# Optimization experiments

Measured on AMD Instinct MI355X. Metric: run time of the kernel, lower is better.

## Reference

```python
import jax, jax.numpy as jnp
import numpy as np

IMG_W = 256
IMG_H = 256
N_PTS = 320
MIN_D = 2.0
MAX_D = 6.0
FOCAL = 2.0          # f = 1/tan(fov/2), fov ~ 53 deg
EPS_EA = 1e-10       # pytorch3d EmissionAbsorption eps
EPS = 1e-8           # module's normalization eps
DENSITY = 0.1        # constant density used when opacity is None


def trilinear_sample(vol, pts):
    """grid_sample-style trilinear, align_corners=True, zero padding.
    vol: (D,H,W); pts: (...,3) local coords (x->W, y->H, z->D) in [-1,1]."""
    D, H, W = vol.shape
    x, y, z = pts[..., 0], pts[..., 1], pts[..., 2]
    ix = (x + 1.0) * 0.5 * (W - 1)
    iy = (y + 1.0) * 0.5 * (H - 1)
    iz = (z + 1.0) * 0.5 * (D - 1)
    x0f, y0f, z0f = jnp.floor(ix), jnp.floor(iy), jnp.floor(iz)
    fx, fy, fz = ix - x0f, iy - y0f, iz - z0f
    x0 = x0f.astype(jnp.int32); x1 = x0 + 1
    y0 = y0f.astype(jnp.int32); y1 = y0 + 1
    z0 = z0f.astype(jnp.int32); z1 = z0 + 1
    out = jnp.zeros_like(ix)
    for zi, wz in ((z0, 1.0 - fz), (z1, fz)):
        for yi, wy in ((y0, 1.0 - fy), (y1, fy)):
            for xi, wx in ((x0, 1.0 - fx), (x1, fx)):
                valid = (xi >= 0) & (xi < W) & (yi >= 0) & (yi < H) & (zi >= 0) & (zi < D)
                v = vol[jnp.clip(zi, 0, D - 1), jnp.clip(yi, 0, H - 1), jnp.clip(xi, 0, W - 1)]
                out = out + jnp.where(valid, v * (wz * wy * wx), 0.0)
    return out


def setup_inputs() -> dict:
    key = jax.random.key(0)
    image3d = jax.random.uniform(key, (1, 1, 256, 256, 256), dtype=jnp.float32)
    R = jnp.eye(3, dtype=jnp.float32)[None]                 # (1,3,3) extrinsic rotation
    T = jnp.array([[0.0, 0.0, 4.0]], dtype=jnp.float32)     # (1,3) camera at z=-4 world
    return {"image3d": image3d, "R": R, "T": T}


def reference(image3d, R, T):
    B, C, D, H, W = image3d.shape
    vol = image3d[:, 0]                                     # (B,D,H,W); RGB repeat -> channels equal
    shape = max(C, D)
    vox = 3.0 / shape
    # --- NDC ray sampling (uniform depths) ---
    yg, xg = jnp.meshgrid(jnp.linspace(-1.0, 1.0, IMG_H),
                          jnp.linspace(-1.0, 1.0, IMG_W), indexing='ij')   # (IH,IW)
    depths = jnp.linspace(MIN_D, MAX_D, N_PTS)
    xcam = xg[..., None] * depths / FOCAL                   # (IH,IW,P)
    ycam = yg[..., None] * depths / FOCAL
    zcam = jnp.broadcast_to(depths, xcam.shape)
    pcam = jnp.stack([xcam, ycam, zcam], axis=-1)           # (IH,IW,P,3)
    # world points: X_cam = X_world @ R + T  =>  X_world = (X_cam - T) @ R^T
    v = pcam[None] - T[:, None, None, None, :]              # (B,IH,IW,P,3)
    pw = jnp.einsum('bhwpj,bkj->bhwpk', v, R)
    # world -> volume local coords (align_corners=True span over voxel centers)
    half = jnp.array([vox * (W - 1) * 0.5, vox * (H - 1) * 0.5, vox * (D - 1) * 0.5], jnp.float32)
    local = pw / half                                       # (B,IH,IW,P,3)
    # --- trilinear gather of features & densities ---
    feat = jax.vmap(trilinear_sample)(vol, local)           # (B,IH,IW,P)
    ones_vol = jnp.ones((D, H, W), jnp.float32)
    sigma = DENSITY * jax.vmap(trilinear_sample, in_axes=(None, 0))(ones_vol, local)
    # --- emission-absorption front-to-back compositing ---
    t = (1.0 + EPS_EA) - sigma
    absorption = jnp.cumprod(t, axis=-1)
    absorption = jnp.concatenate([jnp.ones_like(absorption[..., :1]), absorption[..., :-1]], axis=-1)
    weights = sigma * absorption
    rgb = jnp.sum(weights * feat, axis=-1)                  # (B,IH,IW); RGB channels identical
    # permute(0,3,2,1) then mean over 3 identical RGB channels -> (B,1,IW,IH)
    out = jnp.transpose(rgb, (0, 2, 1))[:, None]
    # norm_type == 'standardized': normalized(standardized(x))
    s = (out - out.mean()) / (jnp.std(out, ddof=1) + EPS)
    out = (s - s.min() + EPS) / (s.max() - s.min() + EPS)
    return out
```

## Files before the change

### kernel.cpp

```cpp
#include <hip/hip_runtime.h>

#define IMG 256
#define NPTS 320
#define NCHUNK 8
#define CHUNK (NPTS / NCHUNK)
#define PIX_PER_BLOCK 64
#define D0 2.0f
#define DSTEP (4.0f / 319.0f)
#define HALFV (765.0f / 512.0f)
#define DENSITY_C 0.1f

__global__ void render_kernel(const float* __restrict__ vol,
                              const float* __restrict__ R,
                              const float* __restrict__ T,
                              float* __restrict__ raw,
                              float* __restrict__ bsum,
                              float* __restrict__ bsumsq,
                              float* __restrict__ bmin,
                              float* __restrict__ bmax) {
  const int lane  = threadIdx.x & 63;
  const int chunk = threadIdx.x >> 6;
  const int pixel = blockIdx.x * PIX_PER_BLOCK + lane;
  const int h = pixel >> 8;
  const int w = pixel & 255;

  const float xh = (w * (2.0f / 255.0f) - 1.0f) * 0.5f;
  const float yh = (h * (2.0f / 255.0f) - 1.0f) * 0.5f;

  const float R00 = R[0], R01 = R[1], R02 = R[2];
  const float R10 = R[3], R11 = R[4], R12 = R[5];
  const float R20 = R[6], R21 = R[7], R22 = R[8];
  const float T0 = T[0], T1 = T[1], T2 = T[2];

  const float S = 127.5f / HALFV;
  const float Cx = R00 * xh + R01 * yh + R02;
  const float Cy = R10 * xh + R11 * yh + R12;
  const float Cz = R20 * xh + R21 * yh + R22;
  const float Kx = -(R00 * T0 + R01 * T1 + R02 * T2);
  const float Ky = -(R10 * T0 + R11 * T1 + R12 * T2);
  const float Kz = -(R20 * T0 + R21 * T1 + R22 * T2);
  const float ax = Cx * S, bx = Kx * S + 127.5f;
  const float ay = Cy * S, by = Ky * S + 127.5f;
  const float az = Cz * S, bz = Kz * S + 127.5f;
  const float ix0 = ax * D0 + bx, dix = ax * DSTEP;
  const float iy0 = ay * D0 + by, diy = ay * DSTEP;
  const float iz0 = az * D0 + bz, diz = az * DSTEP;

  float acc = 0.0f;
  float Tac = 1.0f;
  const int p0 = chunk * CHUNK;

  for (int i = 0; i < CHUNK; ++i) {
    const float pf = (float)(p0 + i);
    const float ix = fmaf(pf, dix, ix0);
    const float iy = fmaf(pf, diy, iy0);
    const float iz = fmaf(pf, diz, iz0);
    if (ix > -1.0f && ix < 256.0f && iy > -1.0f && iy < 256.0f &&
        iz > -1.0f && iz < 256.0f) {
      const float xf = floorf(ix), yf = floorf(iy), zf = floorf(iz);
      const float fx = ix - xf, fy = iy - yf, fz = iz - zf;
      const int x0 = (int)xf, y0 = (int)yf, z0 = (int)zf;
      const float wx0 = (x0 >= 0)   ? 1.0f - fx : 0.0f;
      const float wx1 = (x0 <= 254) ? fx        : 0.0f;
      const float wy0 = (y0 >= 0)   ? 1.0f - fy : 0.0f;
      const float wy1 = (y0 <= 254) ? fy        : 0.0f;
      const float wz0 = (z0 >= 0)   ? 1.0f - fz : 0.0f;
      const float wz1 = (z0 <= 254) ? fz        : 0.0f;
      const int xc0 = max(x0, 0),     xc1 = min(x0 + 1, 255);
      const int yc0 = max(y0, 0),     yc1 = min(y0 + 1, 255);
      const int zc0 = max(z0, 0),     zc1 = min(z0 + 1, 255);
      const int b00 = (zc0 * 256 + yc0) * 256;
      const int b01 = (zc0 * 256 + yc1) * 256;
      const int b10 = (zc1 * 256 + yc0) * 256;
      const int b11 = (zc1 * 256 + yc1) * 256;
      const float v000 = vol[b00 + xc0], v001 = vol[b00 + xc1];
      const float v010 = vol[b01 + xc0], v011 = vol[b01 + xc1];
      const float v100 = vol[b10 + xc0], v101 = vol[b10 + xc1];
      const float v110 = vol[b11 + xc0], v111 = vol[b11 + xc1];
      const float fs =
          wz0 * (wy0 * (wx0 * v000 + wx1 * v001) +
                 wy1 * (wx0 * v010 + wx1 * v011)) +
          wz1 * (wy0 * (wx0 * v100 + wx1 * v101) +
                 wy1 * (wx0 * v110 + wx1 * v111));
      const float wsum  = (wx0 + wx1) * (wy0 + wy1) * (wz0 + wz1);
      const float sigma = DENSITY_C * wsum;
      acc = fmaf(sigma * Tac, fs, acc);
      Tac *= (1.0f + 1e-10f - sigma);
    } else {
      Tac *= (1.0f + 1e-10f);
    }
  }

  __shared__ float lrgb[NCHUNK][PIX_PER_BLOCK];
  __shared__ float lT[NCHUNK][PIX_PER_BLOCK];
  lrgb[chunk][lane] = acc;
  lT[chunk][lane]   = Tac;
  __syncthreads();

  if (threadIdx.x < 64) {
    float a = 0.0f, Tp = 1.0f;
#pragma unroll
    for (int c = 0; c < NCHUNK; ++c) {
      a  = fmaf(Tp, lrgb[c][lane], a);
      Tp *= lT[c][lane];
    }
    raw[pixel] = a;

    float s = a, q = a * a, mn = a, mx = a;
#pragma unroll
    for (int off = 32; off > 0; off >>= 1) {
      s += __shfl_down(s, off, 64);
      q += __shfl_down(q, off, 64);
      mn = fminf(mn, __shfl_down(mn, off, 64));
      mx = fmaxf(mx, __shfl_down(mx, off, 64));
    }
    if (lane == 0) {
      bsum[blockIdx.x]   = s;
      bsumsq[blockIdx.x] = q;
      bmin[blockIdx.x]   = mn;
      bmax[blockIdx.x]   = mx;
    }
  }
}

__global__ void stats_kernel(const float* __restrict__ bsum,
                             const float* __restrict__ bsumsq,
                             const float* __restrict__ bmin,
                             const float* __restrict__ bmax,
                             float* __restrict__ stats) {
  __shared__ double sS[256], sQ[256];
  __shared__ float sMn[256], sMx[256];
  const int t = threadIdx.x;
  double s = 0.0, q = 0.0;
  float mn = 3.4e38f, mx = -3.4e38f;
  for (int i = t; i < 1024; i += 256) {
    s += (double)bsum[i];
    q += (double)bsumsq[i];
    mn = fminf(mn, bmin[i]);
    mx = fmaxf(mx, bmax[i]);
  }
  sS[t] = s; sQ[t] = q; sMn[t] = mn; sMx[t] = mx;
  __syncthreads();
  for (int off = 128; off > 0; off >>= 1) {
    if (t < off) {
      sS[t] += sS[t + off];
      sQ[t] += sQ[t + off];
      sMn[t] = fminf(sMn[t], sMn[t + off]);
      sMx[t] = fmaxf(sMx[t], sMx[t + off]);
    }
    __syncthreads();
  }
  if (t == 0) {
    const double N = 65536.0;
    const double mean = sS[0] / N;
    double var = (sQ[0] - sS[0] * sS[0] / N) / (N - 1.0);
    if (var < 0.0) var = 0.0;
    const float stdeps = (float)sqrt(var) + 1e-8f;
    const float fmean = (float)mean;
    const float smin = (sMn[0] - fmean) / stdeps;
    const float smax = (sMx[0] - fmean) / stdeps;
    stats[0] = fmean;
    stats[1] = 1.0f / stdeps;
    stats[2] = smin;
    stats[3] = 1.0f / (smax - smin + 1e-8f);
  }
}

__global__ void finalize_kernel(const float* __restrict__ raw,
                                const float* __restrict__ stats,
                                float* __restrict__ out) {
  const int o = blockIdx.x * blockDim.x + threadIdx.x;
  const int wq = o >> 8;
  const int hq = o & 255;
  const float mean = stats[0], inv_std = stats[1];
  const float smin = stats[2], inv_range = stats[3];
  const float s = (raw[hq * 256 + wq] - mean) * inv_std;
  out[o] = (s - smin + 1e-8f) * inv_range;
}

extern "C" void kernel_launch(void* const* d_in, const int* in_sizes, int n_in,
                              void* d_out, int out_size, void* d_ws, size_t ws_size,
                              hipStream_t stream) {
  const float* vol = (const float*)d_in[0];
  const float* R   = (const float*)d_in[1];
  const float* T   = (const float*)d_in[2];
  float* out = (float*)d_out;

  float* raw    = (float*)d_ws;
  float* bsum   = raw + 65536;
  float* bsumsq = bsum + 1024;
  float* bmin   = bsumsq + 1024;
  float* bmax   = bmin + 1024;
  float* stats  = bmax + 1024;

  render_kernel<<<1024, 512, 0, stream>>>(vol, R, T, raw, bsum, bsumsq, bmin, bmax);
  stats_kernel<<<1, 256, 0, stream>>>(bsum, bsumsq, bmin, bmax, stats);
  finalize_kernel<<<256, 256, 0, stream>>>(raw, stats, out);
}
```

Baseline: 131.1 us.

## Precompute ray-box intervals for a branch-free interior loop; fuse stats into finalize

Each ray's entry and exit sample indices against the volume are computed analytically with slab tests. Fully-interior samples then run a branchless trilinear loop with no bounds checks or weight masking. Only the boundary samples use the masked path, and samples fully outside are skipped. The stats reduction is also merged into the finalize kernel, with every block redoing the reduction, which removes one launch. The risks are numerical edge cases near the slab margins and the redundant per-block reduction.

```diff
diff --git a/kernel.cpp b/kernel.cpp
--- a/kernel.cpp
+++ b/kernel.cpp
@@ -1,6 +1,5 @@
 #include <hip/hip_runtime.h>
 
-#define IMG 256
 #define NPTS 320
 #define NCHUNK 8
 #define CHUNK (NPTS / NCHUNK)
@@ -10,14 +9,15 @@
 #define HALFV (765.0f / 512.0f)
 #define DENSITY_C 0.1f
 
-__global__ void render_kernel(const float* __restrict__ vol,
-                              const float* __restrict__ R,
-                              const float* __restrict__ T,
-                              float* __restrict__ raw,
-                              float* __restrict__ bsum,
-                              float* __restrict__ bsumsq,
-                              float* __restrict__ bmin,
-                              float* __restrict__ bmax) {
+__global__ __launch_bounds__(512, 8)
+void render_kernel(const float* __restrict__ vol,
+                   const float* __restrict__ R,
+                   const float* __restrict__ T,
+                   float* __restrict__ raw,
+                   float* __restrict__ bsum,
+                   float* __restrict__ bsumsq,
+                   float* __restrict__ bmin,
+                   float* __restrict__ bmax) {
   const int lane  = threadIdx.x & 63;
   const int chunk = threadIdx.x >> 6;
   const int pixel = blockIdx.x * PIX_PER_BLOCK + lane;
@@ -46,12 +46,34 @@
   const float iy0 = ay * D0 + by, diy = ay * DSTEP;
   const float iz0 = az * D0 + bz, diz = az * DSTEP;
 
+  float plo_in = -1e9f, phi_in = 1e9f, plo_out = -1e9f, phi_out = 1e9f;
+  auto slab = [](float a, float b, float L, float H, float& lo, float& hi) {
+    if (fabsf(a) < 1e-5f) {
+      if (b < L || b > H) { lo = 1e9f; hi = -1e9f; }
+    } else {
+      const float p1 = (L - b) / a, p2 = (H - b) / a;
+      lo = fmaxf(lo, fminf(p1, p2));
+      hi = fminf(hi, fmaxf(p1, p2));
+    }
+  };
+  slab(dix, ix0, 0.01f, 254.99f, plo_in, phi_in);
+  slab(diy, iy0, 0.01f, 254.99f, plo_in, phi_in);
+  slab(diz, iz0, 0.01f, 254.99f, plo_in, phi_in);
+  slab(dix, ix0, -1.01f, 256.01f, plo_out, phi_out);
+  slab(diy, iy0, -1.01f, 256.01f, plo_out, phi_out);
+  slab(diz, iz0, -1.01f, 256.01f, plo_out, phi_out);
+
+  const int i_in_lo  = (int)ceilf(fminf(fmaxf(plo_in, 0.0f), 320.0f));
+  const int i_in_hi  = (int)floorf(fminf(fmaxf(phi_in, -1.0f), 319.0f)) + 1;
+  const int i_out_lo = (int)ceilf(fminf(fmaxf(plo_out, 0.0f), 320.0f));
+  const int i_out_hi = (int)floorf(fminf(fmaxf(phi_out, -1.0f), 319.0f)) + 1;
+
   float acc = 0.0f;
   float Tac = 1.0f;
   const int p0 = chunk * CHUNK;
 
-  for (int i = 0; i < CHUNK; ++i) {
-    const float pf = (float)(p0 + i);
+  auto masked_sample = [&](int p) {
+    const float pf = (float)p;
     const float ix = fmaf(pf, dix, ix0);
     const float iy = fmaf(pf, diy, iy0);
     const float iz = fmaf(pf, diz, iz0);
@@ -89,7 +111,42 @@
     } else {
       Tac *= (1.0f + 1e-10f);
     }
+  };
+
+  const int lo_o = max(p0, i_out_lo);
+  const int hi_o = min(p0 + CHUNK, i_out_hi);
+  const int lo_f = min(max(lo_o, i_in_lo), hi_o);
+  const int hi_f = min(max(lo_f, i_in_hi), hi_o);
+
+  for (int p = lo_o; p < lo_f; ++p) masked_sample(p);
+
+#pragma unroll 4
+  for (int p = lo_f; p < hi_f; ++p) {
+    const float pf = (float)p;
+    const float ix = fmaf(pf, dix, ix0);
+    const float iy = fmaf(pf, diy, iy0);
+    const float iz = fmaf(pf, diz, iz0);
+    const int x0 = (int)ix, y0 = (int)iy, z0 = (int)iz;
+    const float fx = ix - (float)x0;
+    const float fy = iy - (float)y0;
+    const float fz = iz - (float)z0;
+    const int base = (z0 << 16) + (y0 << 8) + x0;
+    const float v000 = vol[base],         v001 = vol[base + 1];
+    const float v010 = vol[base + 256],   v011 = vol[base + 257];
+    const float v100 = vol[base + 65536], v101 = vol[base + 65537];
+    const float v110 = vol[base + 65792], v111 = vol[base + 65793];
+    const float c00 = fmaf(fx, v001 - v000, v000);
+    const float c01 = fmaf(fx, v011 - v010, v010);
+    const float c10 = fmaf(fx, v101 - v100, v100);
+    const float c11 = fmaf(fx, v111 - v110, v110);
+    const float c0  = fmaf(fy, c01 - c00, c00);
+    const float c1  = fmaf(fy, c11 - c10, c10);
+    const float fs  = fmaf(fz, c1 - c0, c0);
+    acc = fmaf(Tac * DENSITY_C, fs, acc);
+    Tac *= (1.0f - DENSITY_C);
   }
+
+  for (int p = hi_f; p < hi_o; ++p) masked_sample(p);
 
   __shared__ float lrgb[NCHUNK][PIX_PER_BLOCK];
   __shared__ float lT[NCHUNK][PIX_PER_BLOCK];
@@ -123,25 +180,23 @@
   }
 }
 
-__global__ void stats_kernel(const float* __restrict__ bsum,
-                             const float* __restrict__ bsumsq,
-                             const float* __restrict__ bmin,
-                             const float* __restrict__ bmax,
-                             float* __restrict__ stats) {
-  __shared__ double sS[256], sQ[256];
-  __shared__ float sMn[256], sMx[256];
+__global__ __launch_bounds__(1024)
+void finalize_kernel(const float* __restrict__ raw,
+                     const float* __restrict__ bsum,
+                     const float* __restrict__ bsumsq,
+                     const float* __restrict__ bmin,
+                     const float* __restrict__ bmax,
+                     float* __restrict__ out) {
+  __shared__ double sS[1024];
+  __shared__ double sQ[1024];
+  __shared__ float sMn[1024], sMx[1024];
   const int t = threadIdx.x;
-  double s = 0.0, q = 0.0;
-  float mn = 3.4e38f, mx = -3.4e38f;
-  for (int i = t; i < 1024; i += 256) {
-    s += (double)bsum[i];
-    q += (double)bsumsq[i];
-    mn = fminf(mn, bmin[i]);
-    mx = fmaxf(mx, bmax[i]);
-  }
-  sS[t] = s; sQ[t] = q; sMn[t] = mn; sMx[t] = mx;
+  sS[t] = (double)bsum[t];
+  sQ[t] = (double)bsumsq[t];
+  sMn[t] = bmin[t];
+  sMx[t] = bmax[t];
   __syncthreads();
-  for (int off = 128; off > 0; off >>= 1) {
+  for (int off = 512; off > 0; off >>= 1) {
     if (t < off) {
       sS[t] += sS[t + off];
       sQ[t] += sQ[t + off];
@@ -150,31 +205,22 @@
     }
     __syncthreads();
   }
-  if (t == 0) {
-    const double N = 65536.0;
-    const double mean = sS[0] / N;
-    double var = (sQ[0] - sS[0] * sS[0] / N) / (N - 1.0);
-    if (var < 0.0) var = 0.0;
-    const float stdeps = (float)sqrt(var) + 1e-8f;
-    const float fmean = (float)mean;
-    const float smin = (sMn[0] - fmean) / stdeps;
-    const float smax = (sMx[0] - fmean) / stdeps;
-    stats[0] = fmean;
-    stats[1] = 1.0f / stdeps;
-    stats[2] = smin;
-    stats[3] = 1.0f / (smax - smin + 1e-8f);
-  }
-}
-
-__global__ void finalize_kernel(const float* __restrict__ raw,
-                                const float* __restrict__ stats,
-                                float* __restrict__ out) {
-  const int o = blockIdx.x * blockDim.x + threadIdx.x;
+  const double N = 65536.0;
+  const double sum = sS[0], sumsq = sQ[0];
+  const double mean = sum / N;
+  double var = (sumsq - sum * sum / N) / (N - 1.0);
+  if (var < 0.0) var = 0.0;
+  const float stdeps = (float)sqrt(var) + 1e-8f;
+  const float inv_std = 1.0f / stdeps;
+  const float fmean = (float)mean;
+  const float smin = (sMn[0] - fmean) * inv_std;
+  const float smax = (sMx[0] - fmean) * inv_std;
+  const float inv_range = 1.0f / (smax - smin + 1e-8f);
+
+  const int o = blockIdx.x * 1024 + t;
   const int wq = o >> 8;
   const int hq = o & 255;
-  const float mean = stats[0], inv_std = stats[1];
-  const float smin = stats[2], inv_range = stats[3];
-  const float s = (raw[hq * 256 + wq] - mean) * inv_std;
+  const float s = (raw[hq * 256 + wq] - fmean) * inv_std;
   out[o] = (s - smin + 1e-8f) * inv_range;
 }
 
@@ -191,9 +237,7 @@
   float* bsumsq = bsum + 1024;
   float* bmin   = bsumsq + 1024;
   float* bmax   = bmin + 1024;
-  float* stats  = bmax + 1024;
 
   render_kernel<<<1024, 512, 0, stream>>>(vol, R, T, raw, bsum, bsumsq, bmin, bmax);
-  stats_kernel<<<1, 256, 0, stream>>>(bsum, bsumsq, bmin, bmax, stats);
-  finalize_kernel<<<256, 256, 0, stream>>>(raw, stats, out);
+  finalize_kernel<<<64, 1024, 0, stream>>>(raw, bsum, bsumsq, bmin, bmax, out);
 }
```

New measurement: 125.6 us. -4.2%, faster.
